# Optimization experiments

Hardware: AMD Instinct MI355X
Metric: run time of the kernel (lower is better)

## Reference

```python
import jax, jax.numpy as jnp
import numpy as np

N = 100000   # nodes
E = 1600000  # edges
F = 128      # input node features
H = 128      # hidden channels
G = 512      # graphs in batch
EPS = 1e-5   # BatchNorm eps


def setup_inputs() -> dict:
    key = jax.random.key(0)
    ks = jax.random.split(key, 24)
    x = jax.random.normal(ks[0], (N, F), jnp.float32)
    edge_index = jax.random.randint(ks[1], (2, E), 0, N)
    batch = jnp.sort(jax.random.randint(ks[2], (N,), 0, G))

    def lin_w(k, i, o):
        return jax.random.normal(k, (i, o), jnp.float32) / np.sqrt(i)

    inp = {
        "x": x, "edge_index": edge_index, "batch": batch,
        "W1": lin_w(ks[3], F, H), "b1": jnp.zeros((H,), jnp.float32),
        "g1": jnp.ones((H,), jnp.float32), "be1": jnp.zeros((H,), jnp.float32),
        "m1": 0.1 * jax.random.normal(ks[4], (H,), jnp.float32),
        "v1": jax.random.uniform(ks[5], (H,), jnp.float32) + 0.5,
        "W2": lin_w(ks[6], H, H), "b2": jnp.zeros((H,), jnp.float32),
        "g2": jnp.ones((H,), jnp.float32), "be2": jnp.zeros((H,), jnp.float32),
        "m2": 0.1 * jax.random.normal(ks[7], (H,), jnp.float32),
        "v2": jax.random.uniform(ks[8], (H,), jnp.float32) + 0.5,
        "W3": lin_w(ks[9], H, H), "b3": jnp.zeros((H,), jnp.float32),
        "g3": jnp.ones((H,), jnp.float32), "be3": jnp.zeros((H,), jnp.float32),
        "m3": 0.1 * jax.random.normal(ks[10], (H,), jnp.float32),
        "v3": jax.random.uniform(ks[11], (H,), jnp.float32) + 0.5,
        "Wl": lin_w(ks[12], H, 1), "bl": jnp.zeros((1,), jnp.float32),
    }
    return inp


def _gcn_norm(edge_index):
    # add self-loops, then symmetric normalization deg^-1/2 A_hat deg^-1/2
    loops = jnp.arange(N)
    src = jnp.concatenate([edge_index[0], loops])
    dst = jnp.concatenate([edge_index[1], loops])
    deg = jax.ops.segment_sum(jnp.ones_like(src, jnp.float32), dst, num_segments=N)
    dinv = jax.lax.rsqrt(jnp.maximum(deg, 1.0))
    norm = dinv[src] * dinv[dst]  # [E+N]
    return src, dst, norm


def _gcn_conv(x, W, b, src, dst, norm):
    h = x @ W                                    # [N,H] dense GEMM first (PyG order)
    msg = h[src] * norm[:, None]                 # gather + scale, [E+N,H]
    agg = jax.ops.segment_sum(msg, dst, num_segments=N)  # scatter-add
    return agg + b


def _bn_relu(x, g, be, m, v):
    # inference BatchNorm1d (running stats) + ReLU
    return jax.nn.relu((x - m) * jax.lax.rsqrt(v + EPS) * g + be)


def reference(x, edge_index, batch,
              W1, b1, g1, be1, m1, v1,
              W2, b2, g2, be2, m2, v2,
              W3, b3, g3, be3, m3, v3,
              Wl, bl):
    src, dst, norm = _gcn_norm(edge_index)
    h = _bn_relu(_gcn_conv(x, W1, b1, src, dst, norm), g1, be1, m1, v1)
    h = _bn_relu(_gcn_conv(h, W2, b2, src, dst, norm), g2, be2, m2, v2)
    h = _bn_relu(_gcn_conv(h, W3, b3, src, dst, norm), g3, be3, m3, v3)
    # global mean pool over graphs
    sums = jax.ops.segment_sum(h, batch, num_segments=G)           # [G,H]
    cnt = jax.ops.segment_sum(jnp.ones((N,), jnp.float32), batch, num_segments=G)
    pooled = sums / jnp.maximum(cnt, 1.0)[:, None]
    # dropout is identity at inference; final linear
    return pooled @ Wl + bl  # [G,1]
```

## Files before the change

kernel.cpp:

```cpp
#include <hip/hip_runtime.h>
#include <hip/hip_bf16.h>

#define NN 100000
#define NE 1600000
#define HD 128
#define NG 512
#define BN_EPS 1e-5f

#define GEMM_BLOCKS 1563
#define HIST_BLOCKS 6250

typedef __attribute__((ext_vector_type(8))) short short8;
typedef __attribute__((ext_vector_type(4))) float floatx4;

__device__ __forceinline__ ushort f2bf(float f) {
    union { float f; uint u; } v; v.f = f;
    uint r = (v.u + 0x7FFF + ((v.u >> 16) & 1)) >> 16;
    return (ushort)r;
}
__device__ __forceinline__ float bflo(uint u) { union { uint u; float f; } v; v.u = u << 16; return v.f; }
__device__ __forceinline__ float bfhi(uint u) { union { uint u; float f; } v; v.u = u & 0xFFFF0000u; return v.f; }

__global__ void k_prep_all(const float* __restrict__ W1, const float* __restrict__ W2,
                           const float* __restrict__ W3,
                           ushort* __restrict__ Wt1, ushort* __restrict__ Wt2,
                           ushort* __restrict__ Wt3,
                           const float* __restrict__ b1, const float* __restrict__ g1,
                           const float* __restrict__ be1, const float* __restrict__ m1,
                           const float* __restrict__ v1,
                           const float* __restrict__ b2, const float* __restrict__ g2,
                           const float* __restrict__ be2, const float* __restrict__ m2,
                           const float* __restrict__ v2,
                           const float* __restrict__ b3, const float* __restrict__ g3,
                           const float* __restrict__ be3, const float* __restrict__ m3,
                           const float* __restrict__ v3,
                           float* scale1, float* shift1, float* scale2, float* shift2,
                           float* scale3, float* shift3,
                           const int* __restrict__ batch, int* __restrict__ gstart,
                           int* __restrict__ indeg) {
    int blk = blockIdx.x, tid = threadIdx.x;
    if (blk < 192) {
        int w = blk >> 6;
        int i = (blk & 63) * 256 + tid;
        const float* W = (w == 0) ? W1 : (w == 1) ? W2 : W3;
        ushort* Wt = (w == 0) ? Wt1 : (w == 1) ? Wt2 : Wt3;
        int k = i >> 7, n = i & 127;
        Wt[n * 128 + k] = f2bf(W[i]);
    } else if (blk < 195) {
        if (tid >= 128) return;
        int l = blk - 192;
        const float *b, *g, *be, *m, *v;
        float *sc, *sh;
        if (l == 0)      { b = b1; g = g1; be = be1; m = m1; v = v1; sc = scale1; sh = shift1; }
        else if (l == 1) { b = b2; g = g2; be = be2; m = m2; v = v2; sc = scale2; sh = shift2; }
        else             { b = b3; g = g3; be = be3; m = m3; v = v3; sc = scale3; sh = shift3; }
        float s = g[tid] * rsqrtf(v[tid] + BN_EPS);
        sc[tid] = s;
        sh[tid] = (b[tid] - m[tid]) * s + be[tid];
    } else if (blk < 198) {
        int g = (blk - 195) * 256 + tid;
        if (g > NG) return;
        if (g == NG) { gstart[NG] = NN; return; }
        int lo = 0, hi = NN;
        while (lo < hi) {
            int mid = (lo + hi) >> 1;
            if (batch[mid] < g) lo = mid + 1; else hi = mid;
        }
        gstart[g] = lo;
    } else {
        int i = (blk - 198) * 256 + tid;
        if (i < NN) indeg[i] = 0;
    }
}

__launch_bounds__(256)
__global__ void k_fused1(const float* __restrict__ x, const ushort* __restrict__ Wt,
                         ushort* __restrict__ hs,
                         const int* __restrict__ dst, int* __restrict__ indeg,
                         int* __restrict__ rank) {
    const int tid = threadIdx.x;
    if (blockIdx.x >= GEMM_BLOCKS) {
        int e = (blockIdx.x - GEMM_BLOCKS) * 256 + tid;
        if (e < NE) rank[e] = atomicAdd(&indeg[dst[e]], 1);
        return;
    }
    const int wave = tid >> 6, lane = tid & 63;
    const int m = lane & 15, kg = lane >> 4;
    const long row0 = (long)blockIdx.x * 64 + wave * 16;

    long arow = row0 + m;
    long arc = arow < NN ? arow : (NN - 1);
    const float* xf = x + arc * 128;
    short8 a[4];
#pragma unroll
    for (int s = 0; s < 4; ++s) {
        float4 f0 = *(const float4*)(xf + s * 32 + kg * 8);
        float4 f1 = *(const float4*)(xf + s * 32 + kg * 8 + 4);
        short8 t;
        t[0] = (short)f2bf(f0.x); t[1] = (short)f2bf(f0.y);
        t[2] = (short)f2bf(f0.z); t[3] = (short)f2bf(f0.w);
        t[4] = (short)f2bf(f1.x); t[5] = (short)f2bf(f1.y);
        t[6] = (short)f2bf(f1.z); t[7] = (short)f2bf(f1.w);
        a[s] = t;
    }

    floatx4 acc[8];
#pragma unroll
    for (int ct = 0; ct < 8; ++ct) acc[ct] = (floatx4){0.f, 0.f, 0.f, 0.f};

#pragma unroll
    for (int s = 0; s < 4; ++s) {
#pragma unroll
        for (int ct = 0; ct < 8; ++ct) {
            short8 b = *(const short8*)(Wt + (ct * 16 + m) * 128 + s * 32 + kg * 8);
            acc[ct] = __builtin_amdgcn_mfma_f32_16x16x32_bf16(a[s], b, acc[ct], 0, 0, 0);
        }
    }

#pragma unroll
    for (int r = 0; r < 4; ++r) {
        long orow = row0 + kg * 4 + r;
        if (orow < NN) {
#pragma unroll
            for (int ct = 0; ct < 8; ++ct)
                hs[orow * 128 + ct * 16 + m] = f2bf(acc[ct][r]);
        }
    }
}

__global__ void k_scan1d(const int* __restrict__ indeg, int* __restrict__ rs,
                         int* __restrict__ aux, float* __restrict__ dinv) {
    __shared__ int s[256];
    int t = threadIdx.x;
    int base = blockIdx.x * 1024 + t * 4;
    int v0 = 0, v1 = 0, v2 = 0, v3 = 0;
    if (base + 0 < NN) v0 = indeg[base + 0];
    if (base + 1 < NN) v1 = indeg[base + 1];
    if (base + 2 < NN) v2 = indeg[base + 2];
    if (base + 3 < NN) v3 = indeg[base + 3];
    if (base + 0 < NN) dinv[base + 0] = rsqrtf((float)(v0 + 1));
    if (base + 1 < NN) dinv[base + 1] = rsqrtf((float)(v1 + 1));
    if (base + 2 < NN) dinv[base + 2] = rsqrtf((float)(v2 + 1));
    if (base + 3 < NN) dinv[base + 3] = rsqrtf((float)(v3 + 1));
    int tsum = v0 + v1 + v2 + v3;
    s[t] = tsum;
    __syncthreads();
    for (int o = 1; o < 256; o <<= 1) {
        int x = 0;
        if (t >= o) x = s[t - o];
        __syncthreads();
        s[t] += x;
        __syncthreads();
    }
    int excl = s[t] - tsum;
    if (base + 0 < NN) rs[base + 0] = excl;
    if (base + 1 < NN) rs[base + 1] = excl + v0;
    if (base + 2 < NN) rs[base + 2] = excl + v0 + v1;
    if (base + 3 < NN) rs[base + 3] = excl + v0 + v1 + v2;
    if (t == 255) aux[blockIdx.x] = s[255];
}

__global__ void k_scan2(int* __restrict__ aux, int nblk) {
    __shared__ int s[128];
    int t = threadIdx.x;
    int v = (t < nblk) ? aux[t] : 0;
    s[t] = v;
    __syncthreads();
    for (int o = 1; o < 128; o <<= 1) {
        int x = 0;
        if (t >= o) x = s[t - o];
        __syncthreads();
        s[t] += x;
        __syncthreads();
    }
    if (t < nblk) aux[t] = s[t] - v;
}

__global__ void k_scan3(int* __restrict__ rs, const int* __restrict__ aux) {
    int i = blockIdx.x * 256 + threadIdx.x;
    if (i < NN) rs[i] += aux[i >> 10];
    if (i == 0) rs[NN] = NE;
}

__global__ void k_fill(const int* __restrict__ src, const int* __restrict__ dst,
                       const int* __restrict__ rank, const int* __restrict__ rs,
                       int* __restrict__ csr) {
    int e = blockIdx.x * 256 + threadIdx.x;
    if (e >= NE) return;
    csr[rs[dst[e]] + rank[e]] = src[e];
}

#define WT_STRIDE 136
__launch_bounds__(256)
__global__ void k_gemm_l23(const ushort* __restrict__ xb, const ushort* __restrict__ Wt,
                           const float* __restrict__ dinv, ushort* __restrict__ hs) {
    __shared__ ushort sWt[128 * WT_STRIDE];
    const int tid = threadIdx.x;
    for (int i = tid; i < 2048; i += 256) {
        int row = i >> 4, seg = i & 15;
        *(uint4*)&sWt[row * WT_STRIDE + seg * 8] = *(const uint4*)(Wt + row * 128 + seg * 8);
    }
    __syncthreads();

    const int wave = tid >> 6, lane = tid & 63;
    const int m = lane & 15, kg = lane >> 4;
    const long row0 = (long)blockIdx.x * 64 + wave * 16;

    long arow = row0 + m;
    long arc = arow < NN ? arow : (NN - 1);
    short8 a[4];
#pragma unroll
    for (int s = 0; s < 4; ++s)
        a[s] = *(const short8*)(xb + arc * 128 + s * 32 + kg * 8);

    floatx4 acc[8];
#pragma unroll
    for (int ct = 0; ct < 8; ++ct) acc[ct] = (floatx4){0.f, 0.f, 0.f, 0.f};

#pragma unroll
    for (int s = 0; s < 4; ++s) {
#pragma unroll
        for (int ct = 0; ct < 8; ++ct) {
            short8 b = *(const short8*)&sWt[(ct * 16 + m) * WT_STRIDE + s * 32 + kg * 8];
            acc[ct] = __builtin_amdgcn_mfma_f32_16x16x32_bf16(a[s], b, acc[ct], 0, 0, 0);
        }
    }

#pragma unroll
    for (int r = 0; r < 4; ++r) {
        long orow = row0 + kg * 4 + r;
        if (orow < NN) {
            float dd = dinv[orow];
#pragma unroll
            for (int ct = 0; ct < 8; ++ct)
                hs[orow * 128 + ct * 16 + m] = f2bf(acc[ct][r] * dd);
        }
    }
}

template <bool SCALE_SRC>
__global__ void k_gather_bf(const ushort* __restrict__ hs, const int* __restrict__ rs,
                            const int* __restrict__ csr, const float* __restrict__ dinv,
                            const float* __restrict__ scale, const float* __restrict__ shift,
                            ushort* __restrict__ xout) {
    int t = blockIdx.x * 256 + threadIdx.x;
    int d = t >> 4;
    if (d >= NN) return;
    int lane = t & 15;
    int c0 = lane * 8;
    int e0 = rs[d], e1 = rs[d + 1];
    float dd = dinv[d];

    uint4 sv = *(const uint4*)(hs + (long)d * 128 + c0);
    float w = SCALE_SRC ? dd : 1.0f;
    float a0 = w * bflo(sv.x), a1 = w * bfhi(sv.x), a2 = w * bflo(sv.y), a3 = w * bfhi(sv.y);
    float a4 = w * bflo(sv.z), a5 = w * bfhi(sv.z), a6 = w * bflo(sv.w), a7 = w * bfhi(sv.w);

    int j = e0;
    for (; j + 1 < e1; j += 2) {
        int s0 = csr[j], s1 = csr[j + 1];
        uint4 v0 = *(const uint4*)(hs + (long)s0 * 128 + c0);
        uint4 v1 = *(const uint4*)(hs + (long)s1 * 128 + c0);
        if (SCALE_SRC) {
            float w0 = dinv[s0], w1 = dinv[s1];
            a0 += w0 * bflo(v0.x) + w1 * bflo(v1.x);
            a1 += w0 * bfhi(v0.x) + w1 * bfhi(v1.x);
            a2 += w0 * bflo(v0.y) + w1 * bflo(v1.y);
            a3 += w0 * bfhi(v0.y) + w1 * bfhi(v1.y);
            a4 += w0 * bflo(v0.z) + w1 * bflo(v1.z);
            a5 += w0 * bfhi(v0.z) + w1 * bfhi(v1.z);
            a6 += w0 * bflo(v0.w) + w1 * bflo(v1.w);
            a7 += w0 * bfhi(v0.w) + w1 * bfhi(v1.w);
        } else {
            a0 += bflo(v0.x) + bflo(v1.x); a1 += bfhi(v0.x) + bfhi(v1.x);
            a2 += bflo(v0.y) + bflo(v1.y); a3 += bfhi(v0.y) + bfhi(v1.y);
            a4 += bflo(v0.z) + bflo(v1.z); a5 += bfhi(v0.z) + bfhi(v1.z);
            a6 += bflo(v0.w) + bflo(v1.w); a7 += bfhi(v0.w) + bfhi(v1.w);
        }
    }
    if (j < e1) {
        int s0 = csr[j];
        uint4 v0 = *(const uint4*)(hs + (long)s0 * 128 + c0);
        float w0 = SCALE_SRC ? dinv[s0] : 1.0f;
        a0 += w0 * bflo(v0.x); a1 += w0 * bfhi(v0.x);
        a2 += w0 * bflo(v0.y); a3 += w0 * bfhi(v0.y);
        a4 += w0 * bflo(v0.z); a5 += w0 * bfhi(v0.z);
        a6 += w0 * bflo(v0.w); a7 += w0 * bfhi(v0.w);
    }

    float4 sca = *(const float4*)(scale + c0);
    float4 scb = *(const float4*)(scale + c0 + 4);
    float4 sha = *(const float4*)(shift + c0);
    float4 shb = *(const float4*)(shift + c0 + 4);
    float r0 = fmaxf(dd * a0 * sca.x + sha.x, 0.f);
    float r1 = fmaxf(dd * a1 * sca.y + sha.y, 0.f);
    float r2 = fmaxf(dd * a2 * sca.z + sha.z, 0.f);
    float r3 = fmaxf(dd * a3 * sca.w + sha.w, 0.f);
    float r4 = fmaxf(dd * a4 * scb.x + shb.x, 0.f);
    float r5 = fmaxf(dd * a5 * scb.y + shb.y, 0.f);
    float r6 = fmaxf(dd * a6 * scb.z + shb.z, 0.f);
    float r7 = fmaxf(dd * a7 * scb.w + shb.w, 0.f);
    uint4 o;
    o.x = (uint)f2bf(r0) | ((uint)f2bf(r1) << 16);
    o.y = (uint)f2bf(r2) | ((uint)f2bf(r3) << 16);
    o.z = (uint)f2bf(r4) | ((uint)f2bf(r5) << 16);
    o.w = (uint)f2bf(r6) | ((uint)f2bf(r7) << 16);
    *(uint4*)(xout + (long)d * 128 + c0) = o;
}

__global__ void k_pool_final2(const ushort* __restrict__ x, const int* __restrict__ gstart,
                              const float* __restrict__ Wl, const float* __restrict__ bl,
                              float* __restrict__ out) {
    __shared__ float red[256];
    int g = blockIdx.x;
    int tid = threadIdx.x;
    int f = tid & 127;
    int half = tid >> 7;
    int i0 = gstart[g], i1 = gstart[g + 1];

    float acc = 0.f;
    for (int i = i0 + half; i < i1; i += 2) {
        union { uint u; float f; } v; v.u = (uint)x[(long)i * 128 + f] << 16;
        acc += v.f;
    }
    red[tid] = acc;
    __syncthreads();
    if (tid < 128) red[tid] = (red[tid] + red[tid + 128]) * Wl[tid];
    __syncthreads();
    for (int o = 64; o > 0; o >>= 1) {
        if (tid < o) red[tid] += red[tid + o];
        __syncthreads();
    }
    if (tid == 0) out[g] = red[0] / fmaxf((float)(i1 - i0), 1.f) + bl[0];
}

extern "C" void kernel_launch(void* const* d_in, const int* in_sizes, int n_in,
                              void* d_out, int out_size, void* d_ws, size_t ws_size,
                              hipStream_t stream) {
    const float* x   = (const float*)d_in[0];
    const int*   ei  = (const int*)d_in[1];
    const int*   bat = (const int*)d_in[2];
    const float* W1  = (const float*)d_in[3];
    const float* b1  = (const float*)d_in[4];
    const float* g1  = (const float*)d_in[5];
    const float* be1 = (const float*)d_in[6];
    const float* m1  = (const float*)d_in[7];
    const float* v1  = (const float*)d_in[8];
    const float* W2  = (const float*)d_in[9];
    const float* b2  = (const float*)d_in[10];
    const float* g2  = (const float*)d_in[11];
    const float* be2 = (const float*)d_in[12];
    const float* m2  = (const float*)d_in[13];
    const float* v2  = (const float*)d_in[14];
    const float* W3  = (const float*)d_in[15];
    const float* b3  = (const float*)d_in[16];
    const float* g3  = (const float*)d_in[17];
    const float* be3 = (const float*)d_in[18];
    const float* m3  = (const float*)d_in[19];
    const float* v3  = (const float*)d_in[20];
    const float* Wl  = (const float*)d_in[21];
    const float* bl  = (const float*)d_in[22];
    float* out = (float*)d_out;

    const int* srcp = ei;
    const int* dstp = ei + NE;

    char* ws = (char*)d_ws;
    size_t off = 0;
    auto alloc = [&](size_t bytes) { char* p = ws + off; off += (bytes + 255) & ~255ULL; return p; };
    float*  dinv   = (float*) alloc(NN * 4);
    int*    indeg  = (int*)   alloc(NN * 4);
    int*    rs     = (int*)   alloc((NN + 1) * 4);
    int*    aux    = (int*)   alloc(128 * 4);
    int*    csr    = (int*)   alloc(NE * 4);
    int*    rank   = (int*)   alloc(NE * 4);
    float*  scale1 = (float*) alloc(HD * 4);
    float*  shift1 = (float*) alloc(HD * 4);
    float*  scale2 = (float*) alloc(HD * 4);
    float*  shift2 = (float*) alloc(HD * 4);
    float*  scale3 = (float*) alloc(HD * 4);
    float*  shift3 = (float*) alloc(HD * 4);
    int*    gstart = (int*)   alloc((NG + 1) * 4);
    ushort* Wt1    = (ushort*)alloc(128 * 128 * 2);
    ushort* Wt2    = (ushort*)alloc(128 * 128 * 2);
    ushort* Wt3    = (ushort*)alloc(128 * 128 * 2);
    ushort* hs     = (ushort*)alloc((size_t)NN * HD * 2);
    ushort* xbuf   = (ushort*)alloc((size_t)NN * HD * 2);

    const int nblk_scan = (NN + 1023) / 1024;
    const int grid_n    = (NN + 255) / 256;
    const int grid_e    = (NE + 255) / 256;
    const int gath_grid = (NN * 16 + 255) / 256;

    k_prep_all<<<198 + grid_n, 256, 0, stream>>>(W1, W2, W3, Wt1, Wt2, Wt3,
                                        b1, g1, be1, m1, v1,
                                        b2, g2, be2, m2, v2,
                                        b3, g3, be3, m3, v3,
                                        scale1, shift1, scale2, shift2, scale3, shift3,
                                        bat, gstart, indeg);

    k_fused1<<<GEMM_BLOCKS + HIST_BLOCKS, 256, 0, stream>>>(x, Wt1, hs, dstp, indeg, rank);

    k_scan1d<<<nblk_scan, 256, 0, stream>>>(indeg, rs, aux, dinv);
    k_scan2<<<1, 128, 0, stream>>>(aux, nblk_scan);
    k_scan3<<<grid_n, 256, 0, stream>>>(rs, aux);
    k_fill<<<grid_e, 256, 0, stream>>>(srcp, dstp, rank, rs, csr);

    k_gather_bf<true><<<gath_grid, 256, 0, stream>>>(hs, rs, csr, dinv, scale1, shift1, xbuf);
    k_gemm_l23<<<GEMM_BLOCKS, 256, 0, stream>>>(xbuf, Wt2, dinv, hs);
    k_gather_bf<false><<<gath_grid, 256, 0, stream>>>(hs, rs, csr, dinv, scale2, shift2, xbuf);
    k_gemm_l23<<<GEMM_BLOCKS, 256, 0, stream>>>(xbuf, Wt3, dinv, hs);
    k_gather_bf<false><<<gath_grid, 256, 0, stream>>>(hs, rs, csr, dinv, scale3, shift3, xbuf);

    k_pool_final2<<<NG, 256, 0, stream>>>(xbuf, gstart, Wl, bl, out);
}
```

Baseline: 513.7 us.

## Fuse neighbor gather into following layer GEMM and merge scan passes

Aggregated node rows from the sparse gather are now staged in shared memory and fed straight into the MFMA GEMM of the next layer. This removes the intermediate xbuf write and read plus two kernel launches, and uses ping-pong hs buffers. The weight matrix is now read from global memory (L2/L1) instead of being staged in LDS. The 64-row blocks may also reduce gather parallelism and occupancy. The second and third scan kernels are merged so that each block rescans the block sums itself.

```diff
diff --git a/kernel.cpp b/kernel.cpp
--- a/kernel.cpp
+++ b/kernel.cpp
@@ -160,25 +160,23 @@
     if (t == 255) aux[blockIdx.x] = s[255];
 }
 
-__global__ void k_scan2(int* __restrict__ aux, int nblk) {
+__global__ void k_scan23(int* __restrict__ rs, const int* __restrict__ aux, int nblk) {
     __shared__ int s[128];
     int t = threadIdx.x;
-    int v = (t < nblk) ? aux[t] : 0;
-    s[t] = v;
+    if (t < 128) s[t] = (t < nblk) ? aux[t] : 0;
     __syncthreads();
     for (int o = 1; o < 128; o <<= 1) {
         int x = 0;
-        if (t >= o) x = s[t - o];
+        if (t < 128 && t >= o) x = s[t - o];
         __syncthreads();
-        s[t] += x;
+        if (t < 128) s[t] += x;
         __syncthreads();
     }
-    if (t < nblk) aux[t] = s[t] - v;
-}
-
-__global__ void k_scan3(int* __restrict__ rs, const int* __restrict__ aux) {
-    int i = blockIdx.x * 256 + threadIdx.x;
-    if (i < NN) rs[i] += aux[i >> 10];
+    int i = blockIdx.x * 256 + t;
+    if (i < NN) {
+        int b = i >> 10;
+        rs[i] += b ? s[b - 1] : 0;
+    }
     if (i == 0) rs[NN] = NE;
 }
 
@@ -190,28 +188,92 @@
     csr[rs[dst[e]] + rank[e]] = src[e];
 }
 
-#define WT_STRIDE 136
+#define SR_STRIDE 136
+template <bool SCALE_SRC>
 __launch_bounds__(256)
-__global__ void k_gemm_l23(const ushort* __restrict__ xb, const ushort* __restrict__ Wt,
-                           const float* __restrict__ dinv, ushort* __restrict__ hs) {
-    __shared__ ushort sWt[128 * WT_STRIDE];
+__global__ void k_gather_gemm(const ushort* __restrict__ hs_in, const int* __restrict__ rs,
+                              const int* __restrict__ csr, const float* __restrict__ dinv,
+                              const float* __restrict__ scale, const float* __restrict__ shift,
+                              const ushort* __restrict__ Wt, ushort* __restrict__ hs_out) {
+    __shared__ ushort sRows[64 * SR_STRIDE];
     const int tid = threadIdx.x;
-    for (int i = tid; i < 2048; i += 256) {
-        int row = i >> 4, seg = i & 15;
-        *(uint4*)&sWt[row * WT_STRIDE + seg * 8] = *(const uint4*)(Wt + row * 128 + seg * 8);
+    const long row0 = (long)blockIdx.x * 64;
+    const int lane16 = tid & 15;
+    const int c0 = lane16 * 8;
+
+#pragma unroll
+    for (int it = 0; it < 4; ++it) {
+        int dloc = it * 16 + (tid >> 4);
+        long d = row0 + dloc;
+        long dc = d < NN ? d : (NN - 1);
+        int e0 = rs[dc], e1 = rs[dc + 1];
+        float dd = dinv[dc];
+
+        uint4 sv = *(const uint4*)(hs_in + dc * 128 + c0);
+        float w = SCALE_SRC ? dd : 1.0f;
+        float a0 = w * bflo(sv.x), a1 = w * bfhi(sv.x), a2 = w * bflo(sv.y), a3 = w * bfhi(sv.y);
+        float a4 = w * bflo(sv.z), a5 = w * bfhi(sv.z), a6 = w * bflo(sv.w), a7 = w * bfhi(sv.w);
+
+        int j = e0;
+        for (; j + 1 < e1; j += 2) {
+            int s0 = csr[j], s1 = csr[j + 1];
+            uint4 v0 = *(const uint4*)(hs_in + (long)s0 * 128 + c0);
+            uint4 v1 = *(const uint4*)(hs_in + (long)s1 * 128 + c0);
+            if (SCALE_SRC) {
+                float w0 = dinv[s0], w1 = dinv[s1];
+                a0 += w0 * bflo(v0.x) + w1 * bflo(v1.x);
+                a1 += w0 * bfhi(v0.x) + w1 * bfhi(v1.x);
+                a2 += w0 * bflo(v0.y) + w1 * bflo(v1.y);
+                a3 += w0 * bfhi(v0.y) + w1 * bfhi(v1.y);
+                a4 += w0 * bflo(v0.z) + w1 * bflo(v1.z);
+                a5 += w0 * bfhi(v0.z) + w1 * bfhi(v1.z);
+                a6 += w0 * bflo(v0.w) + w1 * bflo(v1.w);
+                a7 += w0 * bfhi(v0.w) + w1 * bfhi(v1.w);
+            } else {
+                a0 += bflo(v0.x) + bflo(v1.x); a1 += bfhi(v0.x) + bfhi(v1.x);
+                a2 += bflo(v0.y) + bflo(v1.y); a3 += bfhi(v0.y) + bfhi(v1.y);
+                a4 += bflo(v0.z) + bflo(v1.z); a5 += bfhi(v0.z) + bfhi(v1.z);
+                a6 += bflo(v0.w) + bflo(v1.w); a7 += bfhi(v0.w) + bfhi(v1.w);
+            }
+        }
+        if (j < e1) {
+            int s0 = csr[j];
+            uint4 v0 = *(const uint4*)(hs_in + (long)s0 * 128 + c0);
+            float w0 = SCALE_SRC ? dinv[s0] : 1.0f;
+            a0 += w0 * bflo(v0.x); a1 += w0 * bfhi(v0.x);
+            a2 += w0 * bflo(v0.y); a3 += w0 * bfhi(v0.y);
+            a4 += w0 * bflo(v0.z); a5 += w0 * bfhi(v0.z);
+            a6 += w0 * bflo(v0.w); a7 += w0 * bfhi(v0.w);
+        }
+
+        float4 sca = *(const float4*)(scale + c0);
+        float4 scb = *(const float4*)(scale + c0 + 4);
+        float4 sha = *(const float4*)(shift + c0);
+        float4 shb = *(const float4*)(shift + c0 + 4);
+        float r0 = fmaxf(dd * a0 * sca.x + sha.x, 0.f);
+        float r1 = fmaxf(dd * a1 * sca.y + sha.y, 0.f);
+        float r2 = fmaxf(dd * a2 * sca.z + sha.z, 0.f);
+        float r3 = fmaxf(dd * a3 * sca.w + sha.w, 0.f);
+        float r4 = fmaxf(dd * a4 * scb.x + shb.x, 0.f);
+        float r5 = fmaxf(dd * a5 * scb.y + shb.y, 0.f);
+        float r6 = fmaxf(dd * a6 * scb.z + shb.z, 0.f);
+        float r7 = fmaxf(dd * a7 * scb.w + shb.w, 0.f);
+        uint4 o;
+        o.x = (uint)f2bf(r0) | ((uint)f2bf(r1) << 16);
+        o.y = (uint)f2bf(r2) | ((uint)f2bf(r3) << 16);
+        o.z = (uint)f2bf(r4) | ((uint)f2bf(r5) << 16);
+        o.w = (uint)f2bf(r6) | ((uint)f2bf(r7) << 16);
+        *(uint4*)&sRows[dloc * SR_STRIDE + c0] = o;
     }
     __syncthreads();
 
     const int wave = tid >> 6, lane = tid & 63;
     const int m = lane & 15, kg = lane >> 4;
-    const long row0 = (long)blockIdx.x * 64 + wave * 16;
-
-    long arow = row0 + m;
-    long arc = arow < NN ? arow : (NN - 1);
+
     short8 a[4];
 #pragma unroll
     for (int s = 0; s < 4; ++s)
-        a[s] = *(const short8*)(xb + arc * 128 + s * 32 + kg * 8);
+        a[s] = *(const short8*)&sRows[(wave * 16 + m) * SR_STRIDE + s * 32 + kg * 8];
 
     floatx4 acc[8];
 #pragma unroll
@@ -221,24 +283,23 @@
     for (int s = 0; s < 4; ++s) {
 #pragma unroll
         for (int ct = 0; ct < 8; ++ct) {
-            short8 b = *(const short8*)&sWt[(ct * 16 + m) * WT_STRIDE + s * 32 + kg * 8];
+            short8 b = *(const short8*)(Wt + (ct * 16 + m) * 128 + s * 32 + kg * 8);
             acc[ct] = __builtin_amdgcn_mfma_f32_16x16x32_bf16(a[s], b, acc[ct], 0, 0, 0);
         }
     }
 
 #pragma unroll
     for (int r = 0; r < 4; ++r) {
-        long orow = row0 + kg * 4 + r;
+        long orow = row0 + wave * 16 + kg * 4 + r;
         if (orow < NN) {
             float dd = dinv[orow];
 #pragma unroll
             for (int ct = 0; ct < 8; ++ct)
-                hs[orow * 128 + ct * 16 + m] = f2bf(acc[ct][r] * dd);
-        }
-    }
-}
-
-template <bool SCALE_SRC>
+                hs_out[orow * 128 + ct * 16 + m] = f2bf(acc[ct][r] * dd);
+        }
+    }
+}
+
 __global__ void k_gather_bf(const ushort* __restrict__ hs, const int* __restrict__ rs,
                             const int* __restrict__ csr, const float* __restrict__ dinv,
                             const float* __restrict__ scale, const float* __restrict__ shift,
@@ -252,40 +313,26 @@
     float dd = dinv[d];
 
     uint4 sv = *(const uint4*)(hs + (long)d * 128 + c0);
-    float w = SCALE_SRC ? dd : 1.0f;
-    float a0 = w * bflo(sv.x), a1 = w * bfhi(sv.x), a2 = w * bflo(sv.y), a3 = w * bfhi(sv.y);
-    float a4 = w * bflo(sv.z), a5 = w * bfhi(sv.z), a6 = w * bflo(sv.w), a7 = w * bfhi(sv.w);
+    float a0 = bflo(sv.x), a1 = bfhi(sv.x), a2 = bflo(sv.y), a3 = bfhi(sv.y);
+    float a4 = bflo(sv.z), a5 = bfhi(sv.z), a6 = bflo(sv.w), a7 = bfhi(sv.w);
 
     int j = e0;
     for (; j + 1 < e1; j += 2) {
         int s0 = csr[j], s1 = csr[j + 1];
         uint4 v0 = *(const uint4*)(hs + (long)s0 * 128 + c0);
         uint4 v1 = *(const uint4*)(hs + (long)s1 * 128 + c0);
-        if (SCALE_SRC) {
-            float w0 = dinv[s0], w1 = dinv[s1];
-            a0 += w0 * bflo(v0.x) + w1 * bflo(v1.x);
-            a1 += w0 * bfhi(v0.x) + w1 * bfhi(v1.x);
-            a2 += w0 * bflo(v0.y) + w1 * bflo(v1.y);
-            a3 += w0 * bfhi(v0.y) + w1 * bfhi(v1.y);
-            a4 += w0 * bflo(v0.z) + w1 * bflo(v1.z);
-            a5 += w0 * bfhi(v0.z) + w1 * bfhi(v1.z);
-            a6 += w0 * bflo(v0.w) + w1 * bflo(v1.w);
-            a7 += w0 * bfhi(v0.w) + w1 * bfhi(v1.w);
-        } else {
-            a0 += bflo(v0.x) + bflo(v1.x); a1 += bfhi(v0.x) + bfhi(v1.x);
-            a2 += bflo(v0.y) + bflo(v1.y); a3 += bfhi(v0.y) + bfhi(v1.y);
-            a4 += bflo(v0.z) + bflo(v1.z); a5 += bfhi(v0.z) + bfhi(v1.z);
-            a6 += bflo(v0.w) + bflo(v1.w); a7 += bfhi(v0.w) + bfhi(v1.w);
-        }
+        a0 += bflo(v0.x) + bflo(v1.x); a1 += bfhi(v0.x) + bfhi(v1.x);
+        a2 += bflo(v0.y) + bflo(v1.y); a3 += bfhi(v0.y) + bfhi(v1.y);
+        a4 += bflo(v0.z) + bflo(v1.z); a5 += bfhi(v0.z) + bfhi(v1.z);
+        a6 += bflo(v0.w) + bflo(v1.w); a7 += bfhi(v0.w) + bfhi(v1.w);
     }
     if (j < e1) {
         int s0 = csr[j];
         uint4 v0 = *(const uint4*)(hs + (long)s0 * 128 + c0);
-        float w0 = SCALE_SRC ? dinv[s0] : 1.0f;
-        a0 += w0 * bflo(v0.x); a1 += w0 * bfhi(v0.x);
-        a2 += w0 * bflo(v0.y); a3 += w0 * bfhi(v0.y);
-        a4 += w0 * bflo(v0.z); a5 += w0 * bfhi(v0.z);
-        a6 += w0 * bflo(v0.w); a7 += w0 * bfhi(v0.w);
+        a0 += bflo(v0.x); a1 += bfhi(v0.x);
+        a2 += bflo(v0.y); a3 += bfhi(v0.y);
+        a4 += bflo(v0.z); a5 += bfhi(v0.z);
+        a6 += bflo(v0.w); a7 += bfhi(v0.w);
     }
 
     float4 sca = *(const float4*)(scale + c0);
@@ -384,7 +431,8 @@
     ushort* Wt1    = (ushort*)alloc(128 * 128 * 2);
     ushort* Wt2    = (ushort*)alloc(128 * 128 * 2);
     ushort* Wt3    = (ushort*)alloc(128 * 128 * 2);
-    ushort* hs     = (ushort*)alloc((size_t)NN * HD * 2);
+    ushort* hsA    = (ushort*)alloc((size_t)NN * HD * 2);
+    ushort* hsB    = (ushort*)alloc((size_t)NN * HD * 2);
     ushort* xbuf   = (ushort*)alloc((size_t)NN * HD * 2);
 
     const int nblk_scan = (NN + 1023) / 1024;
@@ -399,18 +447,17 @@
                                         scale1, shift1, scale2, shift2, scale3, shift3,
                                         bat, gstart, indeg);
 
-    k_fused1<<<GEMM_BLOCKS + HIST_BLOCKS, 256, 0, stream>>>(x, Wt1, hs, dstp, indeg, rank);
+    k_fused1<<<GEMM_BLOCKS + HIST_BLOCKS, 256, 0, stream>>>(x, Wt1, hsA, dstp, indeg, rank);
 
     k_scan1d<<<nblk_scan, 256, 0, stream>>>(indeg, rs, aux, dinv);
-    k_scan2<<<1, 128, 0, stream>>>(aux, nblk_scan);
-    k_scan3<<<grid_n, 256, 0, stream>>>(rs, aux);
+    k_scan23<<<grid_n, 256, 0, stream>>>(rs, aux, nblk_scan);
     k_fill<<<grid_e, 256, 0, stream>>>(srcp, dstp, rank, rs, csr);
 
-    k_gather_bf<true><<<gath_grid, 256, 0, stream>>>(hs, rs, csr, dinv, scale1, shift1, xbuf);
-    k_gemm_l23<<<GEMM_BLOCKS, 256, 0, stream>>>(xbuf, Wt2, dinv, hs);
-    k_gather_bf<false><<<gath_grid, 256, 0, stream>>>(hs, rs, csr, dinv, scale2, shift2, xbuf);
-    k_gemm_l23<<<GEMM_BLOCKS, 256, 0, stream>>>(xbuf, Wt3, dinv, hs);
-    k_gather_bf<false><<<gath_grid, 256, 0, stream>>>(hs, rs, csr, dinv, scale3, shift3, xbuf);
+    k_gather_gemm<true><<<GEMM_BLOCKS, 256, 0, stream>>>(hsA, rs, csr, dinv,
+                                                         scale1, shift1, Wt2, hsB);
+    k_gather_gemm<false><<<GEMM_BLOCKS, 256, 0, stream>>>(hsB, rs, csr, dinv,
+                                                          scale2, shift2, Wt3, hsA);
+    k_gather_bf<<<gath_grid, 256, 0, stream>>>(hsA, rs, csr, dinv, scale3, shift3, xbuf);
 
     k_pool_final2<<<NG, 256, 0, stream>>>(xbuf, gstart, Wl, bl, out);
 }
```

After: 558.2 us. 8.7% more time.
